# Performance work log

Hardware: AMD Instinct MI355X
Metric: run time of the kernel (lower is better)

Reference implementation:

```python
import jax, jax.numpy as jnp
import numpy as np

B, S, D, H = 2, 2048, 1024, 16  # batch, seq_len, model dim, heads


def setup_inputs() -> dict:
    key = jax.random.key(0)
    ks = jax.random.split(key, 5)
    return {
        "x": jax.random.normal(ks[0], (B, S, D), jnp.float32),
        "idx": jax.random.randint(ks[1], (B,), 0, S),
        "weight": jnp.float32(0.5),
        "attn_forcing": 1,  # static python flag
        "w_qkv": jax.random.normal(ks[2], (D, 3 * D), jnp.float32) * 0.02,
        "b_qkv": jnp.zeros((3 * D,), jnp.float32),
        "w_proj": jax.random.normal(ks[3], (D, D), jnp.float32) * 0.02,
        "b_proj": jnp.zeros((D,), jnp.float32),
    }


def reference(x, idx, weight, attn_forcing, w_qkv, b_qkv, w_proj, b_proj):
    Bx, Sx, Dm = x.shape
    dh = Dm // H
    # qkv projection (Conv1D: x @ w + b)
    qkv = x @ w_qkv + b_qkv  # [B,S,3D]
    q, k, v = jnp.split(qkv, 3, axis=-1)
    q = q.reshape(Bx, Sx, H, dh).transpose(0, 2, 1, 3)  # [B,H,S,dh]
    k = k.reshape(Bx, Sx, H, dh).transpose(0, 2, 1, 3)
    v = v.reshape(Bx, Sx, H, dh).transpose(0, 2, 1, 3)
    alen = jnp.arange(Sx)
    mask = (alen[None, :] <= alen[:, None]).astype(x.dtype)  # [S,S] causal
    w = jnp.einsum('bhqd,bhkd->bhqk', q, k) / jnp.asarray(np.sqrt(dh), x.dtype)
    w = w * mask + jnp.asarray(-1e9, x.dtype) * (1 - mask)
    w = jax.nn.softmax(w, axis=-1)
    if attn_forcing:
        # post-softmax forcing reweight: positions >= idx scaled by weight, then renorm
        a = jnp.where(alen[None, :] >= idx[:, None], weight, jnp.asarray(1.0, x.dtype))  # [B,S]
        w = w * a[:, None, None, :]
        w = w / jnp.sum(w, axis=-1, keepdims=True)
    out = jnp.einsum('bhqk,bhkd->bhqd', w, v)  # [B,H,S,dh]
    out = out.transpose(0, 2, 1, 3).reshape(Bx, Sx, Dm)  # merge heads
    return out @ w_proj + b_proj
```

## Files before the change

kernel.cpp:

```cpp
#include <hip/hip_runtime.h>


typedef __attribute__((ext_vector_type(8))) short short8;
typedef __attribute__((ext_vector_type(4))) float f32x4;

#define MFMA_B16(a, b, c) __builtin_amdgcn_mfma_f32_16x16x32_bf16(a, b, c, 0, 0, 0)

#if __has_builtin(__builtin_amdgcn_exp2f)
#define EXP2(x) __builtin_amdgcn_exp2f(x)
#else
#define EXP2(x) exp2f(x)
#endif

static __device__ __forceinline__ unsigned short f2bf(float f) {
    union { float f; unsigned int u; } v;
    v.f = f;
    unsigned int r = (v.u + 0x7fffu + ((v.u >> 16) & 1u)) >> 16;
    return (unsigned short)r;
}

static __device__ __forceinline__ unsigned int pk_bf16(float a, float b) {
#if __has_builtin(__builtin_amdgcn_cvt_pk_bf16_f32)
    typedef __bf16 bf2 __attribute__((ext_vector_type(2)));
    union { bf2 v; unsigned int u; } c;
    c.v = __builtin_amdgcn_cvt_pk_bf16_f32(a, b);
    return c.u;
#else
    return (unsigned int)f2bf(a) | ((unsigned int)f2bf(b) << 16);
#endif
}

static __device__ __forceinline__ void gl_lds16(const void* g, void* l) {
    __builtin_amdgcn_global_load_lds(
        (const __attribute__((address_space(1))) unsigned int*)g,
        (__attribute__((address_space(3))) unsigned int*)l, 16, 0, 0);
}

__global__ __launch_bounds__(256) void prep_kernel(const float4* __restrict__ x,
                                                   ushort4* __restrict__ xb,
                                                   const float* __restrict__ wqkv,
                                                   unsigned short* __restrict__ wqkvT,
                                                   const float* __restrict__ wproj,
                                                   unsigned short* __restrict__ wprojT) {
    const int bid = blockIdx.x;
    if (bid < 4096) {
        int i = bid * 256 + threadIdx.x;
        float4 v = x[i];
        ushort4 o;
        o.x = f2bf(v.x); o.y = f2bf(v.y); o.z = f2bf(v.z); o.w = f2bf(v.w);
        xb[i] = o;
        return;
    }
    __shared__ float t[32][33];
    const float* in;
    unsigned short* out;
    int R, C, bx, by;
    if (bid < 4096 + 3072) {
        int g = bid - 4096;
        in = wqkv; out = wqkvT; R = 1024; C = 3072;
        bx = g % 96; by = g / 96;
    } else {
        int g = bid - 7168;
        in = wproj; out = wprojT; R = 1024; C = 1024;
        bx = g & 31; by = g >> 5;
    }
    const int c0 = bx * 32, r0 = by * 32;
    const int xx = threadIdx.x & 31, yy0 = threadIdx.x >> 5;
    #pragma unroll
    for (int yy = yy0; yy < 32; yy += 8)
        t[yy][xx] = in[(size_t)(r0 + yy) * C + (c0 + xx)];
    __syncthreads();
    #pragma unroll
    for (int yy = yy0; yy < 32; yy += 8)
        out[(size_t)(c0 + yy) * R + (r0 + xx)] = f2bf(t[xx][yy]);
}

__global__ __launch_bounds__(256) void gemm_qkv_kernel(const unsigned short* __restrict__ A,
                                                       const unsigned short* __restrict__ Bt,
                                                       const float* __restrict__ bias,
                                                       unsigned short* __restrict__ q,
                                                       unsigned short* __restrict__ k,
                                                       unsigned short* __restrict__ vT) {
    __shared__ unsigned short As[128 * 64];
    __shared__ unsigned short Bs[128 * 64];
    const int tid = threadIdx.x;
    const int lane = tid & 63, wave = tid >> 6;
    const int l15 = lane & 15, quad = lane >> 4;
    const int wm = wave >> 1, wn = wave & 1;
    const int row0 = blockIdx.y * 128, col0 = blockIdx.x * 128;
    const int K = 1024;
    const bool isV = (blockIdx.x >= 16);

    int srow[4], scol[4], sdst[4];
    #pragma unroll
    for (int h = 0; h < 4; ++h) {
        int D = h * 256 + wave * 64 + lane;
        srow[h] = D >> 3;
        scol[h] = ((D & 7) ^ (srow[h] & 7)) * 8;
        sdst[h] = (h * 256 + wave * 64) * 8;
    }

    f32x4 acc[4][4] = {};

    for (int kt = 0; kt < K; kt += 64) {
        #pragma unroll
        for (int h = 0; h < 4; ++h) {
            gl_lds16(&A[(size_t)(row0 + srow[h]) * K + kt + scol[h]], &As[sdst[h]]);
            gl_lds16(&Bt[(size_t)(col0 + srow[h]) * K + kt + scol[h]], &Bs[sdst[h]]);
        }
        __syncthreads();
        #pragma unroll
        for (int kk = 0; kk < 2; ++kk) {
            short8 af[4], bf[4];
            #pragma unroll
            for (int i = 0; i < 4; ++i) {
                int r = wm * 64 + i * 16 + l15;
                af[i] = *(const short8*)&As[r * 64 + (((kk * 4 + quad) ^ (r & 7)) * 8)];
            }
            #pragma unroll
            for (int j = 0; j < 4; ++j) {
                int r = wn * 64 + j * 16 + l15;
                bf[j] = *(const short8*)&Bs[r * 64 + (((kk * 4 + quad) ^ (r & 7)) * 8)];
            }
            if (isV) {
                #pragma unroll
                for (int i = 0; i < 4; ++i)
                    #pragma unroll
                    for (int j = 0; j < 4; ++j)
                        acc[i][j] = MFMA_B16(af[i], bf[j], acc[i][j]);
            } else {
                #pragma unroll
                for (int i = 0; i < 4; ++i)
                    #pragma unroll
                    for (int j = 0; j < 4; ++j)
                        acc[i][j] = MFMA_B16(bf[j], af[i], acc[i][j]);
            }
        }
        __syncthreads();
    }

    const int b = row0 >> 11;
    const int s0 = row0 & 2047;
    const float* bb = bias + col0 + wn * 64;

    if (!isV) {
        const int which = blockIdx.x >> 3;
        unsigned short* dst = which ? k : q;
        const float scale = which ? 1.0f : 0.1803368867f;
        const int hh = ((blockIdx.x & 7) << 1) + wn;
        #pragma unroll
        for (int i = 0; i < 4; ++i) {
            const int s = s0 + wm * 64 + i * 16 + l15;
            unsigned short* drow = dst + ((size_t)((b * 16 + hh) * 2048 + s)) * 64;
            #pragma unroll
            for (int j = 0; j < 4; ++j) {
                float4 b4 = ((const float4*)bb)[j * 4 + quad];
                uint2 pv;
                pv.x = pk_bf16((acc[i][j][0] + b4.x) * scale, (acc[i][j][1] + b4.y) * scale);
                pv.y = pk_bf16((acc[i][j][2] + b4.z) * scale, (acc[i][j][3] + b4.w) * scale);
                *(uint2*)&drow[j * 16 + quad * 4] = pv;
            }
        }
    } else {
        const int hh = ((blockIdx.x - 16) << 1) + wn;
        #pragma unroll
        for (int j = 0; j < 4; ++j) {
            const int d = j * 16 + l15;
            const float bv = bb[d];
            unsigned short* drow = vT + ((size_t)((b * 16 + hh) * 64 + d)) * 2048 + s0;
            #pragma unroll
            for (int i = 0; i < 4; ++i) {
                uint2 pv;
                pv.x = pk_bf16(acc[i][j][0] + bv, acc[i][j][1] + bv);
                pv.y = pk_bf16(acc[i][j][2] + bv, acc[i][j][3] + bv);
                *(uint2*)&drow[wm * 64 + i * 16 + quad * 4] = pv;
            }
        }
    }
}

__global__ __launch_bounds__(256) void gemm_proj_kernel(const unsigned short* __restrict__ A,
                                                        const unsigned short* __restrict__ Bt,
                                                        const float* __restrict__ bias,
                                                        float* __restrict__ out) {
    __shared__ unsigned short As[128 * 64];
    __shared__ unsigned short Bs[64 * 64];
    const int tid = threadIdx.x;
    const int lane = tid & 63, wave = tid >> 6;
    const int l15 = lane & 15, quad = lane >> 4;
    const int wm = wave >> 1, wn = wave & 1;
    const int row0 = blockIdx.y * 128, col0 = blockIdx.x * 64;
    const int K = 1024;

    int srow[4], scol[4], sdst[4];
    #pragma unroll
    for (int h = 0; h < 4; ++h) {
        int D = h * 256 + wave * 64 + lane;
        srow[h] = D >> 3;
        scol[h] = ((D & 7) ^ (srow[h] & 7)) * 8;
        sdst[h] = (h * 256 + wave * 64) * 8;
    }

    f32x4 acc[4][2] = {};

    for (int kt = 0; kt < K; kt += 64) {
        #pragma unroll
        for (int h = 0; h < 4; ++h)
            gl_lds16(&A[(size_t)(row0 + srow[h]) * K + kt + scol[h]], &As[sdst[h]]);
        #pragma unroll
        for (int h = 0; h < 2; ++h)
            gl_lds16(&Bt[(size_t)(col0 + srow[h]) * K + kt + scol[h]], &Bs[sdst[h]]);
        __syncthreads();
        #pragma unroll
        for (int kk = 0; kk < 2; ++kk) {
            short8 af[4], bf[2];
            #pragma unroll
            for (int i = 0; i < 4; ++i) {
                int r = wm * 64 + i * 16 + l15;
                af[i] = *(const short8*)&As[r * 64 + (((kk * 4 + quad) ^ (r & 7)) * 8)];
            }
            #pragma unroll
            for (int j = 0; j < 2; ++j) {
                int r = wn * 32 + j * 16 + l15;
                bf[j] = *(const short8*)&Bs[r * 64 + (((kk * 4 + quad) ^ (r & 7)) * 8)];
            }
            #pragma unroll
            for (int i = 0; i < 4; ++i)
                #pragma unroll
                for (int j = 0; j < 2; ++j)
                    acc[i][j] = MFMA_B16(bf[j], af[i], acc[i][j]);
        }
        __syncthreads();
    }

    const float* bb = bias + col0 + wn * 32;
    #pragma unroll
    for (int i = 0; i < 4; ++i) {
        const int row = row0 + wm * 64 + i * 16 + l15;
        #pragma unroll
        for (int j = 0; j < 2; ++j) {
            float4 b4 = ((const float4*)bb)[j * 4 + quad];
            float4 ov;
            ov.x = acc[i][j][0] + b4.x;
            ov.y = acc[i][j][1] + b4.y;
            ov.z = acc[i][j][2] + b4.z;
            ov.w = acc[i][j][3] + b4.w;
            *(float4*)&out[(size_t)row * 1024 + col0 + wn * 32 + j * 16 + quad * 4] = ov;
        }
    }
}

__global__ __launch_bounds__(512) void attn_kernel(const unsigned short* __restrict__ Q,
                                                   const unsigned short* __restrict__ Kg,
                                                   const unsigned short* __restrict__ Vt,
                                                   const int* __restrict__ idx,
                                                   const float* __restrict__ weight,
                                                   const int* __restrict__ forcing,
                                                   unsigned short* __restrict__ O) {
    __shared__ unsigned short smem[24576];

    const int tid = threadIdx.x;
    const int lane = tid & 63, wave = tid >> 6;
    const int l15 = lane & 15, quad = lane >> 4;
    const int bid = blockIdx.x;
    const int qh = bid >> 8;
    const int rem = bid & 255;
    const int xcd = rem & 7;
    const int head = (rem >> 3) & 3;
    const int g2 = rem >> 5;
    const int p = qh ? (7 - g2) : (8 + g2);
    const int bh = xcd * 4 + head;
    const int tA = 2 * p + 1, tB = 2 * p;
    const int b = bh >> 4, hh = bh & 15;
    const unsigned short* Qb = Q + (size_t)bh * 2048 * 64;
    const unsigned short* Kh = Kg + (size_t)bh * 2048 * 64;
    const unsigned short* Vh = Vt + (size_t)bh * 2048 * 64;

    const int idxb = idx[b];
    const float lw = (forcing[0] != 0) ? __log2f(weight[0]) : 0.0f;

    const int wq = (wave < 4) ? tA : tB;
    const int wg = wave & 3;
    const int q0 = wq * 64 + wg * 16;
    const int qrow = q0 + l15;
    const int nkb = tA + 1;
    const int nkbw = wq + 1;

    const int rS = tid >> 3;
    const int cS8 = ((tid & 7) ^ (rS & 7)) * 8;

    short8 aq0 = *(const short8*)&Qb[(q0 + l15) * 64 + quad * 8];
    short8 aq1 = *(const short8*)&Qb[(q0 + l15) * 64 + 32 + quad * 8];

    const short8 ones8 = {0x3F80, 0x3F80, 0x3F80, 0x3F80, 0x3F80, 0x3F80, 0x3F80, 0x3F80};

    f32x4 o[4] = {};
    f32x4 lsum = {};

    gl_lds16(Kh + (size_t)rS * 64 + cS8,   &smem[tid * 8]);
    gl_lds16(Vh + (size_t)rS * 2048 + cS8, &smem[8192 + tid * 8]);
    __syncthreads();

    unsigned short* const pwb = &smem[16384 + wave * 1024];
    const int pwr = l15 * 64;
    const int pa7 = l15 & 7;

    for (int kb = 0; kb < nkb; ++kb) {
        const int cur = kb & 1;
        const int kbase = kb * 64;
        if (kb + 1 < nkb) {
            const int nb = kbase + 64;
            gl_lds16(Kh + (size_t)(nb + rS) * 64 + cS8,      &smem[(cur ^ 1) * 4096 + tid * 8]);
            gl_lds16(Vh + (size_t)rS * 2048 + nb + cS8,      &smem[8192 + (cur ^ 1) * 4096 + tid * 8]);
        }

        if (kb < nkbw) {
            const unsigned short* KsP = &smem[cur * 4096];
            const unsigned short* VsP = &smem[8192 + cur * 4096];

            const bool fullF = (kbase >= idxb);
            const bool bndF = (!fullF) && (kbase + 63 >= idxb);
            const float zu = fullF ? lw : 0.0f;

            f32x4 sT[4];
            #pragma unroll
            for (int kt = 0; kt < 4; ++kt) {
                const int row = kt * 16 + l15;
                short8 k0 = *(const short8*)&KsP[row * 64 + ((quad ^ (row & 7)) * 8)];
                short8 k1 = *(const short8*)&KsP[row * 64 + (((4 + quad) ^ (row & 7)) * 8)];
                f32x4 z;
                if (!bndF) {
                    z[0] = zu; z[1] = zu; z[2] = zu; z[3] = zu;
                } else {
                    #pragma unroll
                    for (int r = 0; r < 4; ++r)
                        z[r] = (kbase + kt * 16 + quad * 4 + r >= idxb) ? lw : 0.0f;
                }
                z = MFMA_B16(k0, aq0, z);
                z = MFMA_B16(k1, aq1, z);
                sT[kt] = z;
            }

            if (kb == wq) {
                #pragma unroll
                for (int kt = 0; kt < 4; ++kt)
                    #pragma unroll
                    for (int r = 0; r < 4; ++r)
                        if (kbase + kt * 16 + quad * 4 + r > qrow) sT[kt][r] = -3.0e38f;
            }

            #pragma unroll
            for (int kt = 0; kt < 4; ++kt)
                #pragma unroll
                for (int r = 0; r < 4; ++r)
                    sT[kt][r] = EXP2(sT[kt][r]);

            #pragma unroll
            for (int kt = 0; kt < 4; ++kt) {
                unsigned int* pw = (unsigned int*)&pwb[pwr +
                    (((kt * 2 + (quad >> 1)) ^ pa7) * 8) + (quad & 1) * 4];
                pw[0] = pk_bf16(sT[kt][0], sT[kt][1]);
                pw[1] = pk_bf16(sT[kt][2], sT[kt][3]);
            }

            short8 bp0 = *(const short8*)&pwb[pwr + ((quad ^ pa7) * 8)];
            short8 bp1 = *(const short8*)&pwb[pwr + (((4 + quad) ^ pa7) * 8)];

            lsum = MFMA_B16(ones8, bp0, lsum);
            lsum = MFMA_B16(ones8, bp1, lsum);

            #pragma unroll
            for (int dt = 0; dt < 4; ++dt) {
                const int row = dt * 16 + l15;
                short8 vf0 = *(const short8*)&VsP[row * 64 + ((quad ^ (row & 7)) * 8)];
                short8 vf1 = *(const short8*)&VsP[row * 64 + (((4 + quad) ^ (row & 7)) * 8)];
                f32x4 oo = o[dt];
                oo = MFMA_B16(vf0, bp0, oo);
                oo = MFMA_B16(vf1, bp1, oo);
                o[dt] = oo;
            }
        }

        __syncthreads();
    }

    const float inv = 1.0f / lsum[0];
    unsigned short* sc = &smem[wave * 1152];
    #pragma unroll
    for (int dt = 0; dt < 4; ++dt)
        #pragma unroll
        for (int r = 0; r < 4; ++r)
            sc[l15 * 72 + dt * 16 + quad * 4 + r] = f2bf(o[dt][r] * inv);
    const size_t rowoff = ((size_t)(b * 2048 + q0 + l15)) * 1024 + hh * 64;
    #pragma unroll
    for (int h = 0; h < 2; ++h) {
        short8 v8 = *(const short8*)&sc[l15 * 72 + quad * 16 + h * 8];
        *(short8*)&O[rowoff + quad * 16 + h * 8] = v8;
    }
}

extern "C" void kernel_launch(void* const* d_in, const int* in_sizes, int n_in,
                              void* d_out, int out_size, void* d_ws, size_t ws_size,
                              hipStream_t stream) {
    const float* x        = (const float*)d_in[0];
    const int*   idx      = (const int*)d_in[1];
    const float* weight   = (const float*)d_in[2];
    const int*   forcing  = (const int*)d_in[3];
    const float* w_qkv    = (const float*)d_in[4];
    const float* b_qkv    = (const float*)d_in[5];
    const float* w_proj   = (const float*)d_in[6];
    const float* b_proj   = (const float*)d_in[7];
    float* out = (float*)d_out;

    char* ws = (char*)d_ws;
    unsigned short* xb      = (unsigned short*)(ws);
    unsigned short* wqkvT   = (unsigned short*)(ws + 8388608);
    unsigned short* wprojT  = (unsigned short*)(ws + 14680064);
    unsigned short* qbuf    = (unsigned short*)(ws + 16777216);
    unsigned short* kbuf    = (unsigned short*)(ws + 25165824);
    unsigned short* vTbuf   = (unsigned short*)(ws + 33554432);
    unsigned short* attn_out = xb;

    prep_kernel<<<8192, 256, 0, stream>>>((const float4*)x, (ushort4*)xb,
                                          w_qkv, wqkvT, w_proj, wprojT);
    gemm_qkv_kernel<<<dim3(24, 32), 256, 0, stream>>>(xb, wqkvT, b_qkv, qbuf, kbuf, vTbuf);
    attn_kernel<<<512, 512, 0, stream>>>(qbuf, kbuf, vTbuf, idx, weight, forcing, attn_out);
    gemm_proj_kernel<<<dim3(16, 32), 256, 0, stream>>>(attn_out, wprojT, b_proj, out);
}
```

Measured before the change: 183.3 us.

## Double-buffer GEMM LDS tiles, remap blocks per XCD, widen x conversion

Both GEMM kernels now double-buffer their LDS tiles. The next K-tile's global-to-LDS loads are issued before computing on the current tile, so memory latency overlaps with MFMA work. The grids become 1D with an XCD-aware block-to-tile mapping, so blocks on the same XCD share column tiles for L2 locality. The x-to-bf16 prep now converts 8 floats per thread with packed conversion. The loop keeps one barrier per iteration, and the prefetch writes the other buffer while other waves may still be reading the current one. That raises a possible synchronization-hazard concern, and LDS use doubles, which may lower occupancy.

```diff
diff --git a/kernel.cpp b/kernel.cpp
--- a/kernel.cpp
+++ b/kernel.cpp
@@ -37,17 +37,20 @@
 }
 
 __global__ __launch_bounds__(256) void prep_kernel(const float4* __restrict__ x,
-                                                   ushort4* __restrict__ xb,
+                                                   uint4* __restrict__ xb,
                                                    const float* __restrict__ wqkv,
                                                    unsigned short* __restrict__ wqkvT,
                                                    const float* __restrict__ wproj,
                                                    unsigned short* __restrict__ wprojT) {
     const int bid = blockIdx.x;
-    if (bid < 4096) {
+    if (bid < 2048) {
         int i = bid * 256 + threadIdx.x;
-        float4 v = x[i];
-        ushort4 o;
-        o.x = f2bf(v.x); o.y = f2bf(v.y); o.z = f2bf(v.z); o.w = f2bf(v.w);
+        float4 v0 = x[i * 2], v1 = x[i * 2 + 1];
+        uint4 o;
+        o.x = pk_bf16(v0.x, v0.y);
+        o.y = pk_bf16(v0.z, v0.w);
+        o.z = pk_bf16(v1.x, v1.y);
+        o.w = pk_bf16(v1.z, v1.w);
         xb[i] = o;
         return;
     }
@@ -55,12 +58,12 @@
     const float* in;
     unsigned short* out;
     int R, C, bx, by;
-    if (bid < 4096 + 3072) {
-        int g = bid - 4096;
+    if (bid < 2048 + 3072) {
+        int g = bid - 2048;
         in = wqkv; out = wqkvT; R = 1024; C = 3072;
         bx = g % 96; by = g / 96;
     } else {
-        int g = bid - 7168;
+        int g = bid - 5120;
         in = wproj; out = wprojT; R = 1024; C = 1024;
         bx = g & 31; by = g >> 5;
     }
@@ -81,15 +84,18 @@
                                                        unsigned short* __restrict__ q,
                                                        unsigned short* __restrict__ k,
                                                        unsigned short* __restrict__ vT) {
-    __shared__ unsigned short As[128 * 64];
-    __shared__ unsigned short Bs[128 * 64];
+    __shared__ unsigned short As[2][8192];
+    __shared__ unsigned short Bs[2][8192];
     const int tid = threadIdx.x;
     const int lane = tid & 63, wave = tid >> 6;
     const int l15 = lane & 15, quad = lane >> 4;
     const int wm = wave >> 1, wn = wave & 1;
-    const int row0 = blockIdx.y * 128, col0 = blockIdx.x * 128;
+    const int bid = blockIdx.x;
+    const int xcd = bid & 7, jj = bid >> 3;
+    const int col = xcd * 3 + jj % 3;
+    const int row0 = (jj / 3) * 128, col0 = col * 128;
     const int K = 1024;
-    const bool isV = (blockIdx.x >= 16);
+    const bool isV = (col >= 16);
 
     int srow[4], scol[4], sdst[4];
     #pragma unroll
@@ -102,25 +108,35 @@
 
     f32x4 acc[4][4] = {};
 
-    for (int kt = 0; kt < K; kt += 64) {
-        #pragma unroll
-        for (int h = 0; h < 4; ++h) {
-            gl_lds16(&A[(size_t)(row0 + srow[h]) * K + kt + scol[h]], &As[sdst[h]]);
-            gl_lds16(&Bt[(size_t)(col0 + srow[h]) * K + kt + scol[h]], &Bs[sdst[h]]);
-        }
-        __syncthreads();
+    #pragma unroll
+    for (int h = 0; h < 4; ++h) {
+        gl_lds16(&A[(size_t)(row0 + srow[h]) * K + scol[h]], &As[0][sdst[h]]);
+        gl_lds16(&Bt[(size_t)(col0 + srow[h]) * K + scol[h]], &Bs[0][sdst[h]]);
+    }
+    __syncthreads();
+
+    for (int kt = 0; kt < 16; ++kt) {
+        const int cur = kt & 1;
+        if (kt + 1 < 16) {
+            const int ko = (kt + 1) * 64;
+            #pragma unroll
+            for (int h = 0; h < 4; ++h) {
+                gl_lds16(&A[(size_t)(row0 + srow[h]) * K + ko + scol[h]], &As[cur ^ 1][sdst[h]]);
+                gl_lds16(&Bt[(size_t)(col0 + srow[h]) * K + ko + scol[h]], &Bs[cur ^ 1][sdst[h]]);
+            }
+        }
         #pragma unroll
         for (int kk = 0; kk < 2; ++kk) {
             short8 af[4], bf[4];
             #pragma unroll
             for (int i = 0; i < 4; ++i) {
                 int r = wm * 64 + i * 16 + l15;
-                af[i] = *(const short8*)&As[r * 64 + (((kk * 4 + quad) ^ (r & 7)) * 8)];
+                af[i] = *(const short8*)&As[cur][r * 64 + (((kk * 4 + quad) ^ (r & 7)) * 8)];
             }
             #pragma unroll
             for (int j = 0; j < 4; ++j) {
                 int r = wn * 64 + j * 16 + l15;
-                bf[j] = *(const short8*)&Bs[r * 64 + (((kk * 4 + quad) ^ (r & 7)) * 8)];
+                bf[j] = *(const short8*)&Bs[cur][r * 64 + (((kk * 4 + quad) ^ (r & 7)) * 8)];
             }
             if (isV) {
                 #pragma unroll
@@ -144,10 +160,10 @@
     const float* bb = bias + col0 + wn * 64;
 
     if (!isV) {
-        const int which = blockIdx.x >> 3;
+        const int which = col >> 3;
         unsigned short* dst = which ? k : q;
         const float scale = which ? 1.0f : 0.1803368867f;
-        const int hh = ((blockIdx.x & 7) << 1) + wn;
+        const int hh = ((col & 7) << 1) + wn;
         #pragma unroll
         for (int i = 0; i < 4; ++i) {
             const int s = s0 + wm * 64 + i * 16 + l15;
@@ -162,7 +178,7 @@
             }
         }
     } else {
-        const int hh = ((blockIdx.x - 16) << 1) + wn;
+        const int hh = ((col - 16) << 1) + wn;
         #pragma unroll
         for (int j = 0; j < 4; ++j) {
             const int d = j * 16 + l15;
@@ -183,13 +199,16 @@
                                                         const unsigned short* __restrict__ Bt,
                                                         const float* __restrict__ bias,
                                                         float* __restrict__ out) {
-    __shared__ unsigned short As[128 * 64];
-    __shared__ unsigned short Bs[64 * 64];
+    __shared__ unsigned short As[2][8192];
+    __shared__ unsigned short Bs[2][4096];
     const int tid = threadIdx.x;
     const int lane = tid & 63, wave = tid >> 6;
     const int l15 = lane & 15, quad = lane >> 4;
     const int wm = wave >> 1, wn = wave & 1;
-    const int row0 = blockIdx.y * 128, col0 = blockIdx.x * 64;
+    const int bid = blockIdx.x;
+    const int xcd = bid & 7, jj = bid >> 3;
+    const int colb = xcd * 2 + (jj & 1);
+    const int row0 = (jj >> 1) * 128, col0 = colb * 64;
     const int K = 1024;
 
     int srow[4], scol[4], sdst[4];
@@ -203,26 +222,37 @@
 
     f32x4 acc[4][2] = {};
 
-    for (int kt = 0; kt < K; kt += 64) {
-        #pragma unroll
-        for (int h = 0; h < 4; ++h)
-            gl_lds16(&A[(size_t)(row0 + srow[h]) * K + kt + scol[h]], &As[sdst[h]]);
-        #pragma unroll
-        for (int h = 0; h < 2; ++h)
-            gl_lds16(&Bt[(size_t)(col0 + srow[h]) * K + kt + scol[h]], &Bs[sdst[h]]);
-        __syncthreads();
+    #pragma unroll
+    for (int h = 0; h < 4; ++h)
+        gl_lds16(&A[(size_t)(row0 + srow[h]) * K + scol[h]], &As[0][sdst[h]]);
+    #pragma unroll
+    for (int h = 0; h < 2; ++h)
+        gl_lds16(&Bt[(size_t)(col0 + srow[h]) * K + scol[h]], &Bs[0][sdst[h]]);
+    __syncthreads();
+
+    for (int kt = 0; kt < 16; ++kt) {
+        const int cur = kt & 1;
+        if (kt + 1 < 16) {
+            const int ko = (kt + 1) * 64;
+            #pragma unroll
+            for (int h = 0; h < 4; ++h)
+                gl_lds16(&A[(size_t)(row0 + srow[h]) * K + ko + scol[h]], &As[cur ^ 1][sdst[h]]);
+            #pragma unroll
+            for (int h = 0; h < 2; ++h)
+                gl_lds16(&Bt[(size_t)(col0 + srow[h]) * K + ko + scol[h]], &Bs[cur ^ 1][sdst[h]]);
+        }
         #pragma unroll
         for (int kk = 0; kk < 2; ++kk) {
             short8 af[4], bf[2];
             #pragma unroll
             for (int i = 0; i < 4; ++i) {
                 int r = wm * 64 + i * 16 + l15;
-                af[i] = *(const short8*)&As[r * 64 + (((kk * 4 + quad) ^ (r & 7)) * 8)];
+                af[i] = *(const short8*)&As[cur][r * 64 + (((kk * 4 + quad) ^ (r & 7)) * 8)];
             }
             #pragma unroll
             for (int j = 0; j < 2; ++j) {
                 int r = wn * 32 + j * 16 + l15;
-                bf[j] = *(const short8*)&Bs[r * 64 + (((kk * 4 + quad) ^ (r & 7)) * 8)];
+                bf[j] = *(const short8*)&Bs[cur][r * 64 + (((kk * 4 + quad) ^ (r & 7)) * 8)];
             }
             #pragma unroll
             for (int i = 0; i < 4; ++i)
@@ -421,9 +451,9 @@
     unsigned short* vTbuf   = (unsigned short*)(ws + 33554432);
     unsigned short* attn_out = xb;
 
-    prep_kernel<<<8192, 256, 0, stream>>>((const float4*)x, (ushort4*)xb,
+    prep_kernel<<<6144, 256, 0, stream>>>((const float4*)x, (uint4*)xb,
                                           w_qkv, wqkvT, w_proj, wprojT);
-    gemm_qkv_kernel<<<dim3(24, 32), 256, 0, stream>>>(xb, wqkvT, b_qkv, qbuf, kbuf, vTbuf);
+    gemm_qkv_kernel<<<768, 256, 0, stream>>>(xb, wqkvT, b_qkv, qbuf, kbuf, vTbuf);
     attn_kernel<<<512, 512, 0, stream>>>(qbuf, kbuf, vTbuf, idx, weight, forcing, attn_out);
-    gemm_proj_kernel<<<dim3(16, 32), 256, 0, stream>>>(attn_out, wprojT, b_proj, out);
-}
+    gemm_proj_kernel<<<512, 256, 0, stream>>>(attn_out, wprojT, b_proj, out);
+}
```

After: 185.1 us. No clear change (+1.0%).

## Process 128-key blocks per attention iteration and widen x conversion loads

Applied to the files above, without the earlier changes.

The attention loop now loads and processes 128 keys per iteration instead of 64, which halves the number of barrier-separated iterations and drops the per-wave skip for the shorter query tile. The final block is causally masked for both query tiles. LDS use grows to roughly 80KB per block, which may cut occupancy, and the B-tile waves now also compute on a block that is entirely masked for them. Separately, the x-to-bf16 prep now converts eight floats per thread using packed conversion, so fewer blocks are launched.

```diff
diff --git a/kernel.cpp b/kernel.cpp
--- a/kernel.cpp
+++ b/kernel.cpp
@@ -37,17 +37,20 @@
 }
 
 __global__ __launch_bounds__(256) void prep_kernel(const float4* __restrict__ x,
-                                                   ushort4* __restrict__ xb,
+                                                   uint4* __restrict__ xb,
                                                    const float* __restrict__ wqkv,
                                                    unsigned short* __restrict__ wqkvT,
                                                    const float* __restrict__ wproj,
                                                    unsigned short* __restrict__ wprojT) {
     const int bid = blockIdx.x;
-    if (bid < 4096) {
+    if (bid < 2048) {
         int i = bid * 256 + threadIdx.x;
-        float4 v = x[i];
-        ushort4 o;
-        o.x = f2bf(v.x); o.y = f2bf(v.y); o.z = f2bf(v.z); o.w = f2bf(v.w);
+        float4 v0 = x[i * 2], v1 = x[i * 2 + 1];
+        uint4 o;
+        o.x = pk_bf16(v0.x, v0.y);
+        o.y = pk_bf16(v0.z, v0.w);
+        o.z = pk_bf16(v1.x, v1.y);
+        o.w = pk_bf16(v1.z, v1.w);
         xb[i] = o;
         return;
     }
@@ -55,12 +58,12 @@
     const float* in;
     unsigned short* out;
     int R, C, bx, by;
-    if (bid < 4096 + 3072) {
-        int g = bid - 4096;
+    if (bid < 2048 + 3072) {
+        int g = bid - 2048;
         in = wqkv; out = wqkvT; R = 1024; C = 3072;
         bx = g % 96; by = g / 96;
     } else {
-        int g = bid - 7168;
+        int g = bid - 5120;
         in = wproj; out = wprojT; R = 1024; C = 1024;
         bx = g & 31; by = g >> 5;
     }
@@ -257,7 +260,7 @@
                                                    const float* __restrict__ weight,
                                                    const int* __restrict__ forcing,
                                                    unsigned short* __restrict__ O) {
-    __shared__ unsigned short smem[24576];
+    __shared__ unsigned short smem[40960];
 
     const int tid = threadIdx.x;
     const int lane = tid & 63, wave = tid >> 6;
@@ -270,7 +273,6 @@
     const int g2 = rem >> 5;
     const int p = qh ? (7 - g2) : (8 + g2);
     const int bh = xcd * 4 + head;
-    const int tA = 2 * p + 1, tB = 2 * p;
     const int b = bh >> 4, hh = bh & 15;
     const unsigned short* Qb = Q + (size_t)bh * 2048 * 64;
     const unsigned short* Kh = Kg + (size_t)bh * 2048 * 64;
@@ -279,12 +281,11 @@
     const int idxb = idx[b];
     const float lw = (forcing[0] != 0) ? __log2f(weight[0]) : 0.0f;
 
-    const int wq = (wave < 4) ? tA : tB;
+    const int wq = 2 * p + ((wave < 4) ? 1 : 0);
     const int wg = wave & 3;
     const int q0 = wq * 64 + wg * 16;
     const int qrow = q0 + l15;
-    const int nkb = tA + 1;
-    const int nkbw = wq + 1;
+    const int nkb = p + 1;
 
     const int rS = tid >> 3;
     const int cS8 = ((tid & 7) ^ (rS & 7)) * 8;
@@ -297,70 +298,77 @@
     f32x4 o[4] = {};
     f32x4 lsum = {};
 
-    gl_lds16(Kh + (size_t)rS * 64 + cS8,   &smem[tid * 8]);
-    gl_lds16(Vh + (size_t)rS * 2048 + cS8, &smem[8192 + tid * 8]);
+    gl_lds16(Kh + (size_t)rS * 64 + cS8,             &smem[tid * 8]);
+    gl_lds16(Kh + (size_t)(64 + rS) * 64 + cS8,      &smem[4096 + tid * 8]);
+    gl_lds16(Vh + (size_t)rS * 2048 + cS8,           &smem[16384 + tid * 8]);
+    gl_lds16(Vh + (size_t)rS * 2048 + 64 + cS8,      &smem[16384 + 4096 + tid * 8]);
     __syncthreads();
 
-    unsigned short* const pwb = &smem[16384 + wave * 1024];
+    unsigned short* const pwb = &smem[32768 + wave * 1024];
     const int pwr = l15 * 64;
     const int pa7 = l15 & 7;
 
     for (int kb = 0; kb < nkb; ++kb) {
         const int cur = kb & 1;
-        const int kbase = kb * 64;
+        const int kbase = kb * 128;
         if (kb + 1 < nkb) {
-            const int nb = kbase + 64;
-            gl_lds16(Kh + (size_t)(nb + rS) * 64 + cS8,      &smem[(cur ^ 1) * 4096 + tid * 8]);
-            gl_lds16(Vh + (size_t)rS * 2048 + nb + cS8,      &smem[8192 + (cur ^ 1) * 4096 + tid * 8]);
-        }
-
-        if (kb < nkbw) {
-            const unsigned short* KsP = &smem[cur * 4096];
-            const unsigned short* VsP = &smem[8192 + cur * 4096];
-
-            const bool fullF = (kbase >= idxb);
-            const bool bndF = (!fullF) && (kbase + 63 >= idxb);
-            const float zu = fullF ? lw : 0.0f;
-
-            f32x4 sT[4];
-            #pragma unroll
-            for (int kt = 0; kt < 4; ++kt) {
-                const int row = kt * 16 + l15;
-                short8 k0 = *(const short8*)&KsP[row * 64 + ((quad ^ (row & 7)) * 8)];
-                short8 k1 = *(const short8*)&KsP[row * 64 + (((4 + quad) ^ (row & 7)) * 8)];
-                f32x4 z;
-                if (!bndF) {
-                    z[0] = zu; z[1] = zu; z[2] = zu; z[3] = zu;
-                } else {
-                    #pragma unroll
-                    for (int r = 0; r < 4; ++r)
-                        z[r] = (kbase + kt * 16 + quad * 4 + r >= idxb) ? lw : 0.0f;
-                }
-                z = MFMA_B16(k0, aq0, z);
-                z = MFMA_B16(k1, aq1, z);
-                sT[kt] = z;
-            }
-
-            if (kb == wq) {
-                #pragma unroll
-                for (int kt = 0; kt < 4; ++kt)
-                    #pragma unroll
-                    for (int r = 0; r < 4; ++r)
-                        if (kbase + kt * 16 + quad * 4 + r > qrow) sT[kt][r] = -3.0e38f;
-            }
-
-            #pragma unroll
-            for (int kt = 0; kt < 4; ++kt)
+            const int nb = kbase + 128;
+            gl_lds16(Kh + (size_t)(nb + rS) * 64 + cS8,      &smem[(cur ^ 1) * 8192 + tid * 8]);
+            gl_lds16(Kh + (size_t)(nb + 64 + rS) * 64 + cS8, &smem[(cur ^ 1) * 8192 + 4096 + tid * 8]);
+            gl_lds16(Vh + (size_t)rS * 2048 + nb + cS8,      &smem[16384 + (cur ^ 1) * 8192 + tid * 8]);
+            gl_lds16(Vh + (size_t)rS * 2048 + nb + 64 + cS8, &smem[16384 + (cur ^ 1) * 8192 + 4096 + tid * 8]);
+        }
+
+        const unsigned short* KsP = &smem[cur * 8192];
+        const unsigned short* VsP = &smem[16384 + cur * 8192];
+
+        const bool fullF = (kbase >= idxb);
+        const bool bndF = (!fullF) && (kbase + 127 >= idxb);
+        const float zu = fullF ? lw : 0.0f;
+
+        f32x4 sT[8];
+        #pragma unroll
+        for (int kt = 0; kt < 8; ++kt) {
+            const int lr = (kt & 3) * 16 + l15;
+            const unsigned short* Kp = KsP + (kt >> 2) * 4096;
+            short8 k0 = *(const short8*)&Kp[lr * 64 + ((quad ^ (lr & 7)) * 8)];
+            short8 k1 = *(const short8*)&Kp[lr * 64 + (((4 + quad) ^ (lr & 7)) * 8)];
+            f32x4 z;
+            if (!bndF) {
+                z[0] = zu; z[1] = zu; z[2] = zu; z[3] = zu;
+            } else {
                 #pragma unroll
                 for (int r = 0; r < 4; ++r)
-                    sT[kt][r] = EXP2(sT[kt][r]);
-
+                    z[r] = (kbase + kt * 16 + quad * 4 + r >= idxb) ? lw : 0.0f;
+            }
+            z = MFMA_B16(k0, aq0, z);
+            z = MFMA_B16(k1, aq1, z);
+            sT[kt] = z;
+        }
+
+        if (kb == nkb - 1) {
+            #pragma unroll
+            for (int kt = 0; kt < 8; ++kt)
+                #pragma unroll
+                for (int r = 0; r < 4; ++r)
+                    if (kbase + kt * 16 + quad * 4 + r > qrow) sT[kt][r] = -3.0e38f;
+        }
+
+        #pragma unroll
+        for (int kt = 0; kt < 8; ++kt)
+            #pragma unroll
+            for (int r = 0; r < 4; ++r)
+                sT[kt][r] = EXP2(sT[kt][r]);
+
+        #pragma unroll
+        for (int h = 0; h < 2; ++h) {
             #pragma unroll
             for (int kt = 0; kt < 4; ++kt) {
+                f32x4 s = sT[h * 4 + kt];
                 unsigned int* pw = (unsigned int*)&pwb[pwr +
                     (((kt * 2 + (quad >> 1)) ^ pa7) * 8) + (quad & 1) * 4];
-                pw[0] = pk_bf16(sT[kt][0], sT[kt][1]);
-                pw[1] = pk_bf16(sT[kt][2], sT[kt][3]);
+                pw[0] = pk_bf16(s[0], s[1]);
+                pw[1] = pk_bf16(s[2], s[3]);
             }
 
             short8 bp0 = *(const short8*)&pwb[pwr + ((quad ^ pa7) * 8)];
@@ -369,11 +377,12 @@
             lsum = MFMA_B16(ones8, bp0, lsum);
             lsum = MFMA_B16(ones8, bp1, lsum);
 
+            const unsigned short* Vp = VsP + h * 4096;
             #pragma unroll
             for (int dt = 0; dt < 4; ++dt) {
                 const int row = dt * 16 + l15;
-                short8 vf0 = *(const short8*)&VsP[row * 64 + ((quad ^ (row & 7)) * 8)];
-                short8 vf1 = *(const short8*)&VsP[row * 64 + (((4 + quad) ^ (row & 7)) * 8)];
+                short8 vf0 = *(const short8*)&Vp[row * 64 + ((quad ^ (row & 7)) * 8)];
+                short8 vf1 = *(const short8*)&Vp[row * 64 + (((4 + quad) ^ (row & 7)) * 8)];
                 f32x4 oo = o[dt];
                 oo = MFMA_B16(vf0, bp0, oo);
                 oo = MFMA_B16(vf1, bp1, oo);
@@ -421,7 +430,7 @@
     unsigned short* vTbuf   = (unsigned short*)(ws + 33554432);
     unsigned short* attn_out = xb;
 
-    prep_kernel<<<8192, 256, 0, stream>>>((const float4*)x, (ushort4*)xb,
+    prep_kernel<<<6144, 256, 0, stream>>>((const float4*)x, (uint4*)xb,
                                           w_qkv, wqkvT, w_proj, wprojT);
     gemm_qkv_kernel<<<dim3(24, 32), 256, 0, stream>>>(xb, wqkvT, b_qkv, qbuf, kbuf, vTbuf);
     attn_kernel<<<512, 512, 0, stream>>>(qbuf, kbuf, vTbuf, idx, weight, forcing, attn_out);
```

After: 180.4 us. No clear change (-1.6%).
